# Optimization experiments

Measured on AMD Instinct MI355X. Metric: run time of the kernel, lower is better.

The kernel has to match this reference:

```python
import jax, jax.numpy as jnp
import numpy as np

N = 100000
E = 1600000
NEG_SLOPE = 0.2
EPS = 1e-16


def gat_conv(x, src, dst, W, a_src, a_dst, bias, concat):
    """PyG-style GATConv (dropout in eval mode = identity)."""
    H, C = a_src.shape
    xh = (x @ W).reshape(N, H, C)                      # [N,H,C]
    e_src = jnp.sum(xh * a_src[None], axis=-1)         # [N,H]
    e_dst = jnp.sum(xh * a_dst[None], axis=-1)         # [N,H]
    alpha = jax.nn.leaky_relu(e_src[src] + e_dst[dst], NEG_SLOPE)  # [E,H]
    # segment softmax over incoming edges per destination node
    amax = jax.ops.segment_max(alpha, dst, num_segments=N)
    ea = jnp.exp(alpha - amax[dst])
    denom = jax.ops.segment_sum(ea, dst, num_segments=N)
    att = ea / (denom[dst] + EPS)                      # [E,H]
    msg = xh[src] * att[..., None]                     # [E,H,C] (dominant traffic)
    out = jax.ops.segment_sum(msg, dst, num_segments=N)  # [N,H,C]
    out = out.reshape(N, H * C) if concat else out.mean(axis=1)
    return out + bias


def setup_inputs() -> dict:
    key = jax.random.key(0)
    ks = jax.random.split(key, 8)
    in_dim, hidden, heads, ncls = 128, 16, 8, 40
    s1 = 1.0 / np.sqrt(in_dim)
    s2 = 1.0 / np.sqrt(hidden * heads)
    return {
        "x": jax.random.normal(ks[0], (N, in_dim), jnp.float32),
        "edge_index": jax.random.randint(ks[1], (2, E), 0, N, jnp.int32),
        "W1": jax.random.normal(ks[2], (in_dim, heads * hidden), jnp.float32) * s1,
        "att_src1": jax.random.normal(ks[3], (heads, hidden), jnp.float32) * 0.1,
        "att_dst1": jax.random.normal(ks[4], (heads, hidden), jnp.float32) * 0.1,
        "b1": jnp.zeros((heads * hidden,), jnp.float32),
        "W2": jax.random.normal(ks[5], (heads * hidden, ncls), jnp.float32) * s2,
        "att_src2": jax.random.normal(ks[6], (1, ncls), jnp.float32) * 0.1,
        "att_dst2": jax.random.normal(ks[7], (1, ncls), jnp.float32) * 0.1,
        "b2": jnp.zeros((ncls,), jnp.float32),
    }


def reference(x, edge_index, W1, att_src1, att_dst1, b1, W2, att_src2, att_dst2, b2):
    # add self-loops (PyG GATConv default add_self_loops=True)
    loop = jnp.arange(N, dtype=edge_index.dtype)
    src = jnp.concatenate([edge_index[0], loop])
    dst = jnp.concatenate([edge_index[1], loop])
    # layer 1: concat heads, ELU (dropouts are identity in eval mode)
    h = jax.nn.elu(gat_conv(x, src, dst, W1, att_src1, att_dst1, b1, True))
    # layer 2: single head, mean (concat=False)
    logits = gat_conv(h, src, dst, W2, att_src2, att_dst2, b2, False)
    return logits
```

## Files before the change

### kernel.cpp

```cpp
#include <hip/hip_runtime.h>

#define NEG_SLOPE 0.2f
#define EPSF 1e-16f
#define ABLK 512
#define SHIFT 8
#define SWZ(e)  (((e) << 5) | 0x18)
#define SWZ4(e) (((e) << 5) | 0x1C)

using short8 = __attribute__((ext_vector_type(8))) short;
using f32x4  = __attribute__((ext_vector_type(4))) float;

__device__ __forceinline__ float lrelu_exp(float a) {
    a = (a > 0.f) ? a : NEG_SLOPE * a;
    return __expf(a);
}

__device__ __forceinline__ unsigned short f2bf(float f) {
    unsigned u = __float_as_uint(f);
    u += 0x7fff + ((u >> 16) & 1);
    return (unsigned short)(u >> 16);
}

__device__ __forceinline__ float bf2f(unsigned short b) {
    return __uint_as_float(((unsigned)b) << 16);
}

__device__ __forceinline__ float bf_lo(unsigned pv) { return __uint_as_float(pv << 16); }
__device__ __forceinline__ float bf_hi(unsigned pv) { return __uint_as_float(pv & 0xffff0000u); }

template <int PAT>
__device__ __forceinline__ float swz_f(float v) {
    return __uint_as_float((unsigned)__builtin_amdgcn_ds_swizzle(__float_as_int(v), PAT));
}
template <int PAT>
__device__ __forceinline__ int swz_i(int v) {
    return __builtin_amdgcn_ds_swizzle(v, PAT);
}

__global__ __launch_bounds__(256) void k_ph(const int* __restrict__ ei, int E, int N,
                                            int NBK, int* __restrict__ H,
                                            const float* __restrict__ W1,
                                            const float* __restrict__ W2,
                                            unsigned short* __restrict__ W1s,
                                            unsigned short* __restrict__ W2s) {
    __shared__ int hist[512];
    const int t = threadIdx.x;
    if (blockIdx.x < ABLK) {
        for (int i = t; i < NBK; i += 256) hist[i] = 0;
        __syncthreads();
        const int Et = E + N;
        for (int e = blockIdx.x * 256 + t; e < Et; e += ABLK * 256) {
            int d = (e < E) ? ei[E + e] : (e - E);
            atomicAdd(&hist[d >> SHIFT], 1);
        }
        __syncthreads();
        for (int i = t; i < NBK; i += 256)
            H[(size_t)i * ABLK + blockIdx.x] = hist[i];
        return;
    }
    const int tid = (blockIdx.x - ABLK) * 256 + t;
    if (tid < 16384) {
        const int e  = tid & 7;
        const int l  = (tid >> 3) & 63;
        const int nt = (tid >> 9) & 7;
        const int kt = tid >> 12;
        const int k  = kt * 32 + ((l >> 4) * 8) + e;
        const int n  = nt * 16 + (l & 15);
        const float w = W1[k * 128 + n];
        const unsigned short hi = f2bf(w);
        const unsigned short lo = f2bf(w - bf2f(hi));
        const int idx = (kt * 8 + nt) * 512 + l * 8 + e;
        W1s[idx] = hi;
        W1s[16384 + idx] = lo;
    } else {
        const int t2 = tid - 16384;
        if (t2 >= 6144) return;
        const int e  = t2 & 7;
        const int l  = (t2 >> 3) & 63;
        const int g  = t2 >> 9;
        const int nt = g % 3;
        const int kt = g / 3;
        const int k  = kt * 32 + ((l >> 4) * 8) + e;
        const int n  = nt * 16 + (l & 15);
        const float w = (n < 40) ? W2[k * 40 + n] : 0.f;
        const unsigned short hi = f2bf(w);
        const unsigned short lo = f2bf(w - bf2f(hi));
        const int idx = (kt * 3 + nt) * 512 + l * 8 + e;
        W2s[idx] = hi;
        W2s[6144 + idx] = lo;
    }
}

__global__ __launch_bounds__(512) void k_scanH(int* __restrict__ H, int* __restrict__ BT) {
    __shared__ int sd[512];
    const int t = threadIdx.x;
    int* row = H + (size_t)blockIdx.x * ABLK;
    const int v = row[t];
    sd[t] = v;
    __syncthreads();
    for (int off = 1; off < 512; off <<= 1) {
        int add = (t >= off) ? sd[t - off] : 0;
        __syncthreads();
        sd[t] += add;
        __syncthreads();
    }
    row[t] = sd[t] - v;
    if (t == 511) BT[blockIdx.x] = sd[511];
}

__global__ __launch_bounds__(512) void k_scanBT(const int* __restrict__ BT,
                                                int* __restrict__ BB, int NBK) {
    __shared__ int sd[512];
    const int t = threadIdx.x;
    const int v = (t < NBK) ? BT[t] : 0;
    sd[t] = v;
    __syncthreads();
    for (int off = 1; off < 512; off <<= 1) {
        int add = (t >= off) ? sd[t - off] : 0;
        __syncthreads();
        sd[t] += add;
        __syncthreads();
    }
    if (t < NBK) BB[t] = sd[t] - v;
    if (t == 511) BB[NBK] = sd[511];
}

__global__ __launch_bounds__(256) void k_sm(const int* __restrict__ ei, int E, int N,
                                            int NBK, const int* __restrict__ H,
                                            const int* __restrict__ BB,
                                            unsigned* __restrict__ E2,
                                            const float* __restrict__ x,
                                            const unsigned short* __restrict__ W1s,
                                            unsigned short* __restrict__ xhb) {
    __shared__ unsigned short Bs[32768];
    const int t = threadIdx.x;

    if (blockIdx.x < ABLK) {
        int* cnt  = (int*)Bs;
        int* base = (int*)Bs + 512;
        for (int i = t; i < NBK; i += 256) {
            cnt[i] = 0;
            base[i] = BB[i] + H[(size_t)i * ABLK + blockIdx.x];
        }
        __syncthreads();
        const int Et = E + N;
        for (int e = blockIdx.x * 256 + t; e < Et; e += ABLK * 256) {
            int s, d;
            if (e < E) { s = ei[e]; d = ei[E + e]; }
            else       { s = e - E; d = e - E; }
            const int b = d >> SHIFT;
            const int r = atomicAdd(&cnt[b], 1);
            E2[base[b] + r] = (unsigned)s | ((unsigned)(d & 255) << 24);
        }
        return;
    }

    for (int i = t; i < 4096; i += 256)
        ((uint4*)Bs)[i] = ((const uint4*)W1s)[i];

    const int wm = t >> 6;
    const int l  = t & 63;
    const int wrow0 = (blockIdx.x - ABLK) * 64 + wm * 16;
    const int arow = wrow0 + (l & 15);
    const int rc = (arow < N) ? arow : (N - 1);

    short8 ah[4], al[4];
    #pragma unroll
    for (int kt = 0; kt < 4; ++kt) {
        const float* xp = x + (size_t)rc * 128 + kt * 32 + ((l >> 4) * 8);
        const float4 v0 = ((const float4*)xp)[0];
        const float4 v1 = ((const float4*)xp)[1];
        const float vv[8] = {v0.x, v0.y, v0.z, v0.w, v1.x, v1.y, v1.z, v1.w};
        #pragma unroll
        for (int e = 0; e < 8; ++e) {
            const unsigned short hi = f2bf(vv[e]);
            ((unsigned short*)&ah[kt])[e] = hi;
            ((unsigned short*)&al[kt])[e] = f2bf(vv[e] - bf2f(hi));
        }
    }
    __syncthreads();

    f32x4 acc[8] = {};
    #pragma unroll
    for (int kt = 0; kt < 4; ++kt) {
        #pragma unroll
        for (int nt = 0; nt < 8; ++nt) {
            const short8 bh = *(const short8*)(Bs + (kt * 8 + nt) * 512 + l * 8);
            const short8 bl = *(const short8*)(Bs + 16384 + (kt * 8 + nt) * 512 + l * 8);
            acc[nt] = __builtin_amdgcn_mfma_f32_16x16x32_bf16(ah[kt], bh, acc[nt], 0, 0, 0);
            acc[nt] = __builtin_amdgcn_mfma_f32_16x16x32_bf16(ah[kt], bl, acc[nt], 0, 0, 0);
            acc[nt] = __builtin_amdgcn_mfma_f32_16x16x32_bf16(al[kt], bh, acc[nt], 0, 0, 0);
        }
    }

    const int cl = l & 15;
    const int rbase = wrow0 + ((l >> 4) * 4);
    #pragma unroll
    for (int reg = 0; reg < 4; ++reg) {
        const int orow = rbase + reg;
        if (orow < N) {
            #pragma unroll
            for (int nt = 0; nt < 8; ++nt)
                xhb[(size_t)orow * 128 + nt * 16 + cl] = f2bf(acc[nt][reg]);
        }
    }
}

__global__ __launch_bounds__(256) void k_ce(const unsigned* __restrict__ E2,
                                            const int* __restrict__ BB, int N,
                                            int* __restrict__ deg,
                                            int* __restrict__ rowp,
                                            int* __restrict__ csr, int NBK,
                                            const unsigned short* __restrict__ xhb,
                                            const float* __restrict__ asrc,
                                            const float* __restrict__ adst,
                                            float* __restrict__ es,
                                            float* __restrict__ ed) {
    __shared__ int cnt[256];
    __shared__ int sc[256];
    __shared__ int rp[256];
    __shared__ int fl[256];
    const int t = threadIdx.x;

    if (blockIdx.x >= NBK) {
        const int i = (blockIdx.x - NBK) * 256 + t;
        if (i >= N * 8) return;
        const int h = i & 7;
        const uint4* p = (const uint4*)(xhb + (size_t)i * 16);
        const uint4 q0 = p[0], q1 = p[1];
        const unsigned w[8] = {q0.x, q0.y, q0.z, q0.w, q1.x, q1.y, q1.z, q1.w};
        const float* av = asrc + h * 16;
        const float* bv = adst + h * 16;
        float s = 0.f, d = 0.f;
        #pragma unroll
        for (int j = 0; j < 8; ++j) {
            const float v0 = bf_lo(w[j]);
            const float v1 = bf_hi(w[j]);
            s += v0 * av[2 * j] + v1 * av[2 * j + 1];
            d += v0 * bv[2 * j] + v1 * bv[2 * j + 1];
        }
        es[i] = s; ed[i] = d;
        return;
    }

    const int b = blockIdx.x;
    const int lo = BB[b], hi = BB[b + 1];
    const int base_d = b << SHIFT;
    cnt[t] = 0; fl[t] = 0;
    __syncthreads();
    for (int i = lo + t; i < hi; i += 256)
        atomicAdd(&cnt[E2[i] >> 24], 1);
    __syncthreads();
    const int v = cnt[t];
    sc[t] = v;
    __syncthreads();
    for (int off = 1; off < 256; off <<= 1) {
        int add = (t >= off) ? sc[t - off] : 0;
        __syncthreads();
        sc[t] += add;
        __syncthreads();
    }
    rp[t] = sc[t] - v;
    const int d = base_d + t;
    if (d < N) { deg[d] = v; rowp[d] = lo + rp[t]; }
    __syncthreads();
    for (int i = lo + t; i < hi; i += 256) {
        const unsigned e = E2[i];
        const int ld = e >> 24;
        const int r = atomicAdd(&fl[ld], 1);
        csr[lo + rp[ld] + r] = (int)(e & 0xFFFFFFu);
    }
}

__global__ __launch_bounds__(256) void k_l1(const unsigned short* __restrict__ xhb,
                                            const float* __restrict__ es,
                                            const float* __restrict__ ed,
                                            const int* __restrict__ rowp,
                                            const int* __restrict__ deg,
                                            const int* __restrict__ csr,
                                            const float* __restrict__ b1,
                                            unsigned short* __restrict__ hb, int N) {
    const int wave = threadIdx.x >> 6;
    const int lane = threadIdx.x & 63;
    const int n = blockIdx.x * 4 + wave;
    if (n >= N) return;
    const int hA = lane >> 3;
    const int eA = lane & 7;
    const float edv = ed[n * 8 + hA];
    const int start = rowp[n];
    const int cnt = deg[n];
    const int last = cnt - 1;
    const int lane4 = lane * 4;

    float acc0 = 0.f, acc1 = 0.f, dpart = 0.f;
    const char* xb = (const char*)xhb;

    for (int k = 0; k < cnt; k += 8) {
        const int ke = k + eA;
        const int idx = start + min(ke, last);
        const int s = csr[idx];
        float a = lrelu_exp(es[s * 8 + hA] + edv);
        a = (ke <= last) ? a : 0.f;
        dpart += a;
        const int soff = s << 8;
#define L1E(e) { \
        const float ae = swz_f<SWZ(e)>(a); \
        const int   ro = swz_i<SWZ(e)>(soff); \
        const unsigned pv = *(const unsigned*)(xb + (unsigned)(ro + lane4)); \
        acc0 += ae * bf_lo(pv); \
        acc1 += ae * bf_hi(pv); }
        L1E(0) L1E(1) L1E(2) L1E(3) L1E(4) L1E(5) L1E(6) L1E(7)
#undef L1E
    }
    dpart += __shfl_xor(dpart, 1, 64);
    dpart += __shfl_xor(dpart, 2, 64);
    dpart += __shfl_xor(dpart, 4, 64);

    const float inv = 1.f / (dpart + EPSF);
    const float2 bb = *(const float2*)(b1 + lane * 2);
    float o0 = acc0 * inv + bb.x;
    float o1 = acc1 * inv + bb.y;
    o0 = (o0 > 0.f) ? o0 : expm1f(o0);
    o1 = (o1 > 0.f) ? o1 : expm1f(o1);
    const unsigned pk = (unsigned)f2bf(o0) | ((unsigned)f2bf(o1) << 16);
    *(unsigned*)(hb + (size_t)n * 128 + lane * 2) = pk;
}

__global__ __launch_bounds__(256) void k_mm2(const unsigned short* __restrict__ h,
                                             const unsigned short* __restrict__ W2s,
                                             unsigned short* __restrict__ xh2, int N) {
    __shared__ unsigned short Bs[12288];
    const int t = threadIdx.x;
    for (int i = t; i < 1536; i += 256)
        ((uint4*)Bs)[i] = ((const uint4*)W2s)[i];

    const int wm = t >> 6;
    const int l  = t & 63;
    const int wrow0 = blockIdx.x * 64 + wm * 16;
    const int arow = wrow0 + (l & 15);
    const int rc = (arow < N) ? arow : (N - 1);

    short8 a[4];
    #pragma unroll
    for (int kt = 0; kt < 4; ++kt)
        a[kt] = *(const short8*)(h + (size_t)rc * 128 + kt * 32 + ((l >> 4) * 8));
    __syncthreads();

    f32x4 acc[3] = {};
    #pragma unroll
    for (int kt = 0; kt < 4; ++kt) {
        #pragma unroll
        for (int nt = 0; nt < 3; ++nt) {
            const short8 bh = *(const short8*)(Bs + (kt * 3 + nt) * 512 + l * 8);
            const short8 bl = *(const short8*)(Bs + 6144 + (kt * 3 + nt) * 512 + l * 8);
            acc[nt] = __builtin_amdgcn_mfma_f32_16x16x32_bf16(a[kt], bh, acc[nt], 0, 0, 0);
            acc[nt] = __builtin_amdgcn_mfma_f32_16x16x32_bf16(a[kt], bl, acc[nt], 0, 0, 0);
        }
    }

    const int cl = l & 15;
    const int rbase = wrow0 + ((l >> 4) * 4);
    #pragma unroll
    for (int reg = 0; reg < 4; ++reg) {
        const int orow = rbase + reg;
        if (orow < N) {
            #pragma unroll
            for (int nt = 0; nt < 3; ++nt) {
                const int c = nt * 16 + cl;
                if (c < 40)
                    xh2[(size_t)orow * 64 + c] = f2bf(acc[nt][reg]);
            }
        }
    }
}

__global__ __launch_bounds__(256) void k_esed2(const unsigned short* __restrict__ xh2,
                                               const float* __restrict__ as2,
                                               const float* __restrict__ ad2,
                                               float* __restrict__ es2,
                                               float* __restrict__ ed2, int N) {
    const int n = blockIdx.x * 256 + threadIdx.x;
    if (n >= N) return;
    const unsigned* p = (const unsigned*)(xh2 + (size_t)n * 64);
    float s = 0.f, d = 0.f;
    #pragma unroll
    for (int j = 0; j < 20; ++j) {
        const unsigned w = p[j];
        const float v0 = bf_lo(w);
        const float v1 = bf_hi(w);
        s += v0 * as2[2 * j] + v1 * as2[2 * j + 1];
        d += v0 * ad2[2 * j] + v1 * ad2[2 * j + 1];
    }
    es2[n] = s; ed2[n] = d;
}

__global__ __launch_bounds__(256) void k_l2(const unsigned short* __restrict__ xh2,
                                            const float* __restrict__ es2,
                                            const float* __restrict__ ed2,
                                            const int* __restrict__ rowp,
                                            const int* __restrict__ deg,
                                            const int* __restrict__ csr,
                                            const float* __restrict__ b2,
                                            float* __restrict__ out, int N) {
    const int wave = threadIdx.x >> 6;
    const int lane = threadIdx.x & 63;
    const int half = lane >> 5;
    const int n0 = blockIdx.x * 8 + wave * 2;
    if (n0 >= N) return;
    int n = n0 + half;
    const bool valid = (n < N);
    if (!valid) n = N - 1;
    const float edv = ed2[n];
    const int start = rowp[n];
    const int cnt = deg[n];
    const int last = cnt - 1;
    const int eA = lane & 3;
    const int c2 = lane & 31;
    const int cc4 = ((c2 < 20) ? c2 : 19) * 4;
    const char* xb = (const char*)xh2;
    const int cmax = max(cnt, __shfl_xor(cnt, 32, 64));

    float acc0 = 0.f, acc1 = 0.f, dpart = 0.f;
    for (int k = 0; k < cmax; k += 4) {
        const int ke = k + eA;
        const int idx = start + ((ke <= last) ? ke : last);
        const int s = csr[idx];
        const float a = (ke <= last) ? lrelu_exp(es2[s] + edv) : 0.f;
        dpart += a;
        const int soff = s << 7;
#define L2E(e) { \
        const float ae = swz_f<SWZ4(e)>(a); \
        const int   ro = swz_i<SWZ4(e)>(soff); \
        const unsigned pv = *(const unsigned*)(xb + (unsigned)(ro + cc4)); \
        acc0 += ae * bf_lo(pv); \
        acc1 += ae * bf_hi(pv); }
        L2E(0) L2E(1) L2E(2) L2E(3)
#undef L2E
    }
    dpart += __shfl_xor(dpart, 1, 64);
    dpart += __shfl_xor(dpart, 2, 64);

    if (valid && c2 < 20) {
        const float inv = 1.f / (dpart + EPSF);
        const float2 bb = *(const float2*)(b2 + c2 * 2);
        *(float2*)(out + (size_t)n * 40 + c2 * 2) =
            make_float2(acc0 * inv + bb.x, acc1 * inv + bb.y);
    }
}

extern "C" void kernel_launch(void* const* d_in, const int* in_sizes, int n_in,
                              void* d_out, int out_size, void* d_ws, size_t ws_size,
                              hipStream_t stream) {
    const float* x   = (const float*)d_in[0];
    const int*   ei  = (const int*)d_in[1];
    const float* W1  = (const float*)d_in[2];
    const float* as1 = (const float*)d_in[3];
    const float* ad1 = (const float*)d_in[4];
    const float* b1  = (const float*)d_in[5];
    const float* W2  = (const float*)d_in[6];
    const float* as2 = (const float*)d_in[7];
    const float* ad2 = (const float*)d_in[8];
    const float* b2  = (const float*)d_in[9];
    float* out = (float*)d_out;

    const int N   = in_sizes[0] / 128;
    const int E   = in_sizes[1] / 2;
    const int Et  = E + N;
    const int NBK = (N + 255) >> SHIFT;
    const int GBM = (N + 63) / 64;
    const int EB1 = (N * 8 + 255) / 256;

    char* p = (char*)d_ws;
    unsigned short* W1s = (unsigned short*)p; p += 32768 * 2;
    unsigned short* W2s = (unsigned short*)p; p += 12288 * 2;
    unsigned short* xhb = (unsigned short*)p; p += (size_t)N * 128 * 2;
    float* es1  = (float*)p; p += (size_t)N * 8 * 4;
    float* ed1  = (float*)p; p += (size_t)N * 8 * 4;
    int*   deg  = (int*)p;   p += (size_t)N * 4;
    int*   rowp = (int*)p;   p += (size_t)N * 4;
    int*   csr  = (int*)p;   p += (size_t)Et * 4;
    int*   H    = (int*)p;   p += (size_t)512 * ABLK * 4;
    int*   BT   = (int*)p;   p += 512 * 4;
    int*   BB   = (int*)p;   p += 512 * 4;
    unsigned short* hbuf = (unsigned short*)p; p += (size_t)N * 128 * 2;
    unsigned short* xh2  = (unsigned short*)p; p += (size_t)N * 64 * 2;
    unsigned* E2 = (unsigned*)hbuf;
    float* es2 = es1;
    float* ed2 = ed1;

    k_ph    <<<ABLK + 88,       256, 0, stream>>>(ei, E, N, NBK, H, W1, W2, W1s, W2s);
    k_scanH <<<NBK,             512, 0, stream>>>(H, BT);
    k_scanBT<<<1,               512, 0, stream>>>(BT, BB, NBK);
    k_sm    <<<ABLK + GBM,      256, 0, stream>>>(ei, E, N, NBK, H, BB, E2, x, W1s, xhb);
    k_ce    <<<NBK + EB1,       256, 0, stream>>>(E2, BB, N, deg, rowp, csr, NBK,
                                                  xhb, as1, ad1, es1, ed1);
    k_l1    <<<(N + 3) / 4,     256, 0, stream>>>(xhb, es1, ed1, rowp, deg, csr, b1, hbuf, N);
    k_mm2   <<<GBM,             256, 0, stream>>>(hbuf, W2s, xh2, N);
    k_esed2 <<<(N + 255) / 256, 256, 0, stream>>>(xh2, as2, ad2, es2, ed2, N);
    k_l2    <<<(N + 7) / 8,     256, 0, stream>>>(xh2, es2, ed2, rowp, deg, csr, b2, out, N);
}
```

Before: 219.2 us.

## Fuse layer-2 attention scores into GEMM, widen L1 gathers, amortize W staging

```diff
diff --git a/kernel.cpp b/kernel.cpp
--- a/kernel.cpp
+++ b/kernel.cpp
@@ -4,8 +4,8 @@
 #define EPSF 1e-16f
 #define ABLK 512
 #define SHIFT 8
-#define SWZ(e)  (((e) << 5) | 0x18)
 #define SWZ4(e) (((e) << 5) | 0x1C)
+#define SWB(t)  (((t) << 8) | 0x07)
 
 using short8 = __attribute__((ext_vector_type(8))) short;
 using f32x4  = __attribute__((ext_vector_type(4))) float;
@@ -157,51 +157,55 @@
 
     for (int i = t; i < 4096; i += 256)
         ((uint4*)Bs)[i] = ((const uint4*)W1s)[i];
+    __syncthreads();
 
     const int wm = t >> 6;
     const int l  = t & 63;
-    const int wrow0 = (blockIdx.x - ABLK) * 64 + wm * 16;
-    const int arow = wrow0 + (l & 15);
-    const int rc = (arow < N) ? arow : (N - 1);
-
-    short8 ah[4], al[4];
-    #pragma unroll
-    for (int kt = 0; kt < 4; ++kt) {
-        const float* xp = x + (size_t)rc * 128 + kt * 32 + ((l >> 4) * 8);
-        const float4 v0 = ((const float4*)xp)[0];
-        const float4 v1 = ((const float4*)xp)[1];
-        const float vv[8] = {v0.x, v0.y, v0.z, v0.w, v1.x, v1.y, v1.z, v1.w};
-        #pragma unroll
-        for (int e = 0; e < 8; ++e) {
-            const unsigned short hi = f2bf(vv[e]);
-            ((unsigned short*)&ah[kt])[e] = hi;
-            ((unsigned short*)&al[kt])[e] = f2bf(vv[e] - bf2f(hi));
-        }
-    }
-    __syncthreads();
-
-    f32x4 acc[8] = {};
-    #pragma unroll
-    for (int kt = 0; kt < 4; ++kt) {
-        #pragma unroll
-        for (int nt = 0; nt < 8; ++nt) {
-            const short8 bh = *(const short8*)(Bs + (kt * 8 + nt) * 512 + l * 8);
-            const short8 bl = *(const short8*)(Bs + 16384 + (kt * 8 + nt) * 512 + l * 8);
-            acc[nt] = __builtin_amdgcn_mfma_f32_16x16x32_bf16(ah[kt], bh, acc[nt], 0, 0, 0);
-            acc[nt] = __builtin_amdgcn_mfma_f32_16x16x32_bf16(ah[kt], bl, acc[nt], 0, 0, 0);
-            acc[nt] = __builtin_amdgcn_mfma_f32_16x16x32_bf16(al[kt], bh, acc[nt], 0, 0, 0);
-        }
-    }
-
     const int cl = l & 15;
-    const int rbase = wrow0 + ((l >> 4) * 4);
-    #pragma unroll
-    for (int reg = 0; reg < 4; ++reg) {
-        const int orow = rbase + reg;
-        if (orow < N) {
+    const int blk0 = (blockIdx.x - ABLK) * 256;
+
+    for (int g = 0; g < 4; ++g) {
+        const int wrow0 = blk0 + g * 64 + wm * 16;
+        const int arow = wrow0 + cl;
+        const int rc = (arow < N) ? arow : (N - 1);
+
+        short8 ah[4], al[4];
+        #pragma unroll
+        for (int kt = 0; kt < 4; ++kt) {
+            const float* xp = x + (size_t)rc * 128 + kt * 32 + ((l >> 4) * 8);
+            const float4 v0 = ((const float4*)xp)[0];
+            const float4 v1 = ((const float4*)xp)[1];
+            const float vv[8] = {v0.x, v0.y, v0.z, v0.w, v1.x, v1.y, v1.z, v1.w};
             #pragma unroll
-            for (int nt = 0; nt < 8; ++nt)
-                xhb[(size_t)orow * 128 + nt * 16 + cl] = f2bf(acc[nt][reg]);
+            for (int e = 0; e < 8; ++e) {
+                const unsigned short hi = f2bf(vv[e]);
+                ((unsigned short*)&ah[kt])[e] = hi;
+                ((unsigned short*)&al[kt])[e] = f2bf(vv[e] - bf2f(hi));
+            }
+        }
+
+        f32x4 acc[8] = {};
+        #pragma unroll
+        for (int kt = 0; kt < 4; ++kt) {
+            #pragma unroll
+            for (int nt = 0; nt < 8; ++nt) {
+                const short8 bh = *(const short8*)(Bs + (kt * 8 + nt) * 512 + l * 8);
+                const short8 bl = *(const short8*)(Bs + 16384 + (kt * 8 + nt) * 512 + l * 8);
+                acc[nt] = __builtin_amdgcn_mfma_f32_16x16x32_bf16(ah[kt], bh, acc[nt], 0, 0, 0);
+                acc[nt] = __builtin_amdgcn_mfma_f32_16x16x32_bf16(ah[kt], bl, acc[nt], 0, 0, 0);
+                acc[nt] = __builtin_amdgcn_mfma_f32_16x16x32_bf16(al[kt], bh, acc[nt], 0, 0, 0);
+            }
+        }
+
+        const int rbase = wrow0 + ((l >> 4) * 4);
+        #pragma unroll
+        for (int reg = 0; reg < 4; ++reg) {
+            const int orow = rbase + reg;
+            if (orow < N) {
+                #pragma unroll
+                for (int nt = 0; nt < 8; ++nt)
+                    xhb[(size_t)orow * 128 + nt * 16 + cl] = f2bf(acc[nt][reg]);
+            }
         }
     }
 }
@@ -284,15 +288,17 @@
     const int lane = threadIdx.x & 63;
     const int n = blockIdx.x * 4 + wave;
     if (n >= N) return;
-    const int hA = lane >> 3;
-    const int eA = lane & 7;
+    const int hA = lane & 7;
+    const int eA = lane >> 3;
     const float edv = ed[n * 8 + hA];
     const int start = rowp[n];
     const int cnt = deg[n];
     const int last = cnt - 1;
-    const int lane4 = lane * 4;
-
-    float acc0 = 0.f, acc1 = 0.f, dpart = 0.f;
+    const int q = (lane >> 3) & 3;
+    const int boff = hA * 32 + q * 8;
+
+    float4 acc = make_float4(0.f, 0.f, 0.f, 0.f);
+    float dpart = 0.f;
     const char* xb = (const char*)xhb;
 
     for (int k = 0; k < cnt; k += 8) {
@@ -303,95 +309,116 @@
         a = (ke <= last) ? a : 0.f;
         dpart += a;
         const int soff = s << 8;
-#define L1E(e) { \
-        const float ae = swz_f<SWZ(e)>(a); \
-        const int   ro = swz_i<SWZ(e)>(soff); \
-        const unsigned pv = *(const unsigned*)(xb + (unsigned)(ro + lane4)); \
-        acc0 += ae * bf_lo(pv); \
-        acc1 += ae * bf_hi(pv); }
-        L1E(0) L1E(1) L1E(2) L1E(3) L1E(4) L1E(5) L1E(6) L1E(7)
-#undef L1E
-    }
-    dpart += __shfl_xor(dpart, 1, 64);
-    dpart += __shfl_xor(dpart, 2, 64);
-    dpart += __shfl_xor(dpart, 4, 64);
-
-    const float inv = 1.f / (dpart + EPSF);
-    const float2 bb = *(const float2*)(b1 + lane * 2);
-    float o0 = acc0 * inv + bb.x;
-    float o1 = acc1 * inv + bb.y;
-    o0 = (o0 > 0.f) ? o0 : expm1f(o0);
-    o1 = (o1 > 0.f) ? o1 : expm1f(o1);
-    const unsigned pk = (unsigned)f2bf(o0) | ((unsigned)f2bf(o1) << 16);
-    *(unsigned*)(hb + (size_t)n * 128 + lane * 2) = pk;
+#define L1S(tt) { \
+        const float ae = swz_f<SWB(tt)>(a); \
+        const int   ro = swz_i<SWB(tt)>(soff); \
+        const uint2 pv = *(const uint2*)(xb + (unsigned)(ro + boff)); \
+        acc.x += ae * bf_lo(pv.x); \
+        acc.y += ae * bf_hi(pv.x); \
+        acc.z += ae * bf_lo(pv.y); \
+        acc.w += ae * bf_hi(pv.y); }
+        L1S(0) L1S(1) L1S(2) L1S(3)
+#undef L1S
+    }
+    dpart += __shfl_xor(dpart, 8, 64);
+    dpart += __shfl_xor(dpart, 16, 64);
+    dpart += __shfl_xor(dpart, 32, 64);
+    acc.x += __shfl_xor(acc.x, 32, 64);
+    acc.y += __shfl_xor(acc.y, 32, 64);
+    acc.z += __shfl_xor(acc.z, 32, 64);
+    acc.w += __shfl_xor(acc.w, 32, 64);
+
+    if (lane < 32) {
+        const float inv = 1.f / (dpart + EPSF);
+        const int ch = hA * 16 + q * 4;
+        const float4 bb = *(const float4*)(b1 + ch);
+        float o0 = acc.x * inv + bb.x;
+        float o1 = acc.y * inv + bb.y;
+        float o2 = acc.z * inv + bb.z;
+        float o3 = acc.w * inv + bb.w;
+        o0 = (o0 > 0.f) ? o0 : expm1f(o0);
+        o1 = (o1 > 0.f) ? o1 : expm1f(o1);
+        o2 = (o2 > 0.f) ? o2 : expm1f(o2);
+        o3 = (o3 > 0.f) ? o3 : expm1f(o3);
+        uint2 pk;
+        pk.x = (unsigned)f2bf(o0) | ((unsigned)f2bf(o1) << 16);
+        pk.y = (unsigned)f2bf(o2) | ((unsigned)f2bf(o3) << 16);
+        *(uint2*)(hb + (size_t)n * 128 + ch) = pk;
+    }
 }
 
 __global__ __launch_bounds__(256) void k_mm2(const unsigned short* __restrict__ h,
                                              const unsigned short* __restrict__ W2s,
-                                             unsigned short* __restrict__ xh2, int N) {
+                                             const float* __restrict__ as2,
+                                             const float* __restrict__ ad2,
+                                             unsigned short* __restrict__ xh2,
+                                             float* __restrict__ es2,
+                                             float* __restrict__ ed2, int N) {
     __shared__ unsigned short Bs[12288];
     const int t = threadIdx.x;
     for (int i = t; i < 1536; i += 256)
         ((uint4*)Bs)[i] = ((const uint4*)W2s)[i];
+    __syncthreads();
 
     const int wm = t >> 6;
     const int l  = t & 63;
-    const int wrow0 = blockIdx.x * 64 + wm * 16;
-    const int arow = wrow0 + (l & 15);
-    const int rc = (arow < N) ? arow : (N - 1);
-
-    short8 a[4];
-    #pragma unroll
-    for (int kt = 0; kt < 4; ++kt)
-        a[kt] = *(const short8*)(h + (size_t)rc * 128 + kt * 32 + ((l >> 4) * 8));
-    __syncthreads();
-
-    f32x4 acc[3] = {};
-    #pragma unroll
-    for (int kt = 0; kt < 4; ++kt) {
-        #pragma unroll
-        for (int nt = 0; nt < 3; ++nt) {
-            const short8 bh = *(const short8*)(Bs + (kt * 3 + nt) * 512 + l * 8);
-            const short8 bl = *(const short8*)(Bs + 6144 + (kt * 3 + nt) * 512 + l * 8);
-            acc[nt] = __builtin_amdgcn_mfma_f32_16x16x32_bf16(a[kt], bh, acc[nt], 0, 0, 0);
-            acc[nt] = __builtin_amdgcn_mfma_f32_16x16x32_bf16(a[kt], bl, acc[nt], 0, 0, 0);
-        }
-    }
-
     const int cl = l & 15;
-    const int rbase = wrow0 + ((l >> 4) * 4);
-    #pragma unroll
-    for (int reg = 0; reg < 4; ++reg) {
-        const int orow = rbase + reg;
-        if (orow < N) {
+    const float a0 = as2[cl],      d0v = ad2[cl];
+    const float a1 = as2[16 + cl], d1v = ad2[16 + cl];
+    const float a2 = (cl < 8) ? as2[32 + cl] : 0.f;
+    const float d2v = (cl < 8) ? ad2[32 + cl] : 0.f;
+
+    for (int g = 0; g < 4; ++g) {
+        const int wrow0 = blockIdx.x * 256 + g * 64 + wm * 16;
+        const int arow = wrow0 + cl;
+        const int rc = (arow < N) ? arow : (N - 1);
+
+        short8 a[4];
+        #pragma unroll
+        for (int kt = 0; kt < 4; ++kt)
+            a[kt] = *(const short8*)(h + (size_t)rc * 128 + kt * 32 + ((l >> 4) * 8));
+
+        f32x4 acc[3] = {};
+        #pragma unroll
+        for (int kt = 0; kt < 4; ++kt) {
             #pragma unroll
             for (int nt = 0; nt < 3; ++nt) {
-                const int c = nt * 16 + cl;
-                if (c < 40)
-                    xh2[(size_t)orow * 64 + c] = f2bf(acc[nt][reg]);
+                const short8 bh = *(const short8*)(Bs + (kt * 3 + nt) * 512 + l * 8);
+                const short8 bl = *(const short8*)(Bs + 6144 + (kt * 3 + nt) * 512 + l * 8);
+                acc[nt] = __builtin_amdgcn_mfma_f32_16x16x32_bf16(a[kt], bh, acc[nt], 0, 0, 0);
+                acc[nt] = __builtin_amdgcn_mfma_f32_16x16x32_bf16(a[kt], bl, acc[nt], 0, 0, 0);
             }
         }
-    }
-}
-
-__global__ __launch_bounds__(256) void k_esed2(const unsigned short* __restrict__ xh2,
-                                               const float* __restrict__ as2,
-                                               const float* __restrict__ ad2,
-                                               float* __restrict__ es2,
-                                               float* __restrict__ ed2, int N) {
-    const int n = blockIdx.x * 256 + threadIdx.x;
-    if (n >= N) return;
-    const unsigned* p = (const unsigned*)(xh2 + (size_t)n * 64);
-    float s = 0.f, d = 0.f;
-    #pragma unroll
-    for (int j = 0; j < 20; ++j) {
-        const unsigned w = p[j];
-        const float v0 = bf_lo(w);
-        const float v1 = bf_hi(w);
-        s += v0 * as2[2 * j] + v1 * as2[2 * j + 1];
-        d += v0 * ad2[2 * j] + v1 * ad2[2 * j + 1];
-    }
-    es2[n] = s; ed2[n] = d;
+
+        const int rbase = wrow0 + ((l >> 4) * 4);
+        #pragma unroll
+        for (int reg = 0; reg < 4; ++reg) {
+            const int orow = rbase + reg;
+            if (orow < N) {
+                #pragma unroll
+                for (int nt = 0; nt < 3; ++nt) {
+                    const int c = nt * 16 + cl;
+                    if (c < 40)
+                        xh2[(size_t)orow * 64 + c] = f2bf(acc[nt][reg]);
+                }
+            }
+        }
+
+        #pragma unroll
+        for (int reg = 0; reg < 4; ++reg) {
+            float ps = acc[0][reg] * a0 + acc[1][reg] * a1 + acc[2][reg] * a2;
+            float pd = acc[0][reg] * d0v + acc[1][reg] * d1v + acc[2][reg] * d2v;
+            ps += __shfl_xor(ps, 1, 64); ps += __shfl_xor(ps, 2, 64);
+            ps += __shfl_xor(ps, 4, 64); ps += __shfl_xor(ps, 8, 64);
+            pd += __shfl_xor(pd, 1, 64); pd += __shfl_xor(pd, 2, 64);
+            pd += __shfl_xor(pd, 4, 64); pd += __shfl_xor(pd, 8, 64);
+            const int row = rbase + reg;
+            if (cl == reg && row < N) {
+                es2[row] = ps;
+                ed2[row] = pd;
+            }
+        }
+    }
 }
 
 __global__ __launch_bounds__(256) void k_l2(const unsigned short* __restrict__ xh2,
@@ -463,12 +490,12 @@
     const float* b2  = (const float*)d_in[9];
     float* out = (float*)d_out;
 
-    const int N   = in_sizes[0] / 128;
-    const int E   = in_sizes[1] / 2;
-    const int Et  = E + N;
-    const int NBK = (N + 255) >> SHIFT;
-    const int GBM = (N + 63) / 64;
-    const int EB1 = (N * 8 + 255) / 256;
+    const int N    = in_sizes[0] / 128;
+    const int E    = in_sizes[1] / 2;
+    const int Et   = E + N;
+    const int NBK  = (N + 255) >> SHIFT;
+    const int GB256 = (N + 255) / 256;
+    const int EB1  = (N * 8 + 255) / 256;
 
     char* p = (char*)d_ws;
     unsigned short* W1s = (unsigned short*)p; p += 32768 * 2;
@@ -488,14 +515,13 @@
     float* es2 = es1;
     float* ed2 = ed1;
 
-    k_ph    <<<ABLK + 88,       256, 0, stream>>>(ei, E, N, NBK, H, W1, W2, W1s, W2s);
-    k_scanH <<<NBK,             512, 0, stream>>>(H, BT);
-    k_scanBT<<<1,               512, 0, stream>>>(BT, BB, NBK);
-    k_sm    <<<ABLK + GBM,      256, 0, stream>>>(ei, E, N, NBK, H, BB, E2, x, W1s, xhb);
-    k_ce    <<<NBK + EB1,       256, 0, stream>>>(E2, BB, N, deg, rowp, csr, NBK,
-                                                  xhb, as1, ad1, es1, ed1);
-    k_l1    <<<(N + 3) / 4,     256, 0, stream>>>(xhb, es1, ed1, rowp, deg, csr, b1, hbuf, N);
-    k_mm2   <<<GBM,             256, 0, stream>>>(hbuf, W2s, xh2, N);
-    k_esed2 <<<(N + 255) / 256, 256, 0, stream>>>(xh2, as2, ad2, es2, ed2, N);
-    k_l2    <<<(N + 7) / 8,     256, 0, stream>>>(xh2, es2, ed2, rowp, deg, csr, b2, out, N);
-}
+    k_ph    <<<ABLK + 88,    256, 0, stream>>>(ei, E, N, NBK, H, W1, W2, W1s, W2s);
+    k_scanH <<<NBK,          512, 0, stream>>>(H, BT);
+    k_scanBT<<<1,            512, 0, stream>>>(BT, BB, NBK);
+    k_sm    <<<ABLK + GB256, 256, 0, stream>>>(ei, E, N, NBK, H, BB, E2, x, W1s, xhb);
+    k_ce    <<<NBK + EB1,    256, 0, stream>>>(E2, BB, N, deg, rowp, csr, NBK,
+                                               xhb, as1, ad1, es1, ed1);
+    k_l1    <<<(N + 3) / 4,  256, 0, stream>>>(xhb, es1, ed1, rowp, deg, csr, b1, hbuf, N);
+    k_mm2   <<<GB256,        256, 0, stream>>>(hbuf, W2s, as2, ad2, xh2, es2, ed2, N);
+    k_l2    <<<(N + 7) / 8,  256, 0, stream>>>(xh2, es2, ed2, rowp, deg, csr, b2, out, N);
+}
```

Result: slower. 228.8 us (+4.4%).
